# Performance work log

Hardware: AMD Instinct MI355X
Metric: run time of the kernel (lower is better)

The kernel has to match this reference:

```python
import jax, jax.numpy as jnp
import numpy as np

NUM_EMBEDDINGS = 1024
EMBEDDING_DIM = 64


def setup_inputs() -> dict:
    key = jax.random.key(0)
    kx, kw = jax.random.split(key)
    x = jax.random.normal(kx, (16, 4096, EMBEDDING_DIM), dtype=jnp.float32)
    # torch init: uniform(-1/K, 1/K)
    bound = 1.0 / NUM_EMBEDDINGS
    weight = jax.random.uniform(kw, (NUM_EMBEDDINGS, EMBEDDING_DIM),
                                dtype=jnp.float32, minval=-bound, maxval=bound)
    return {"x": x, "weight": weight}


def reference(x, weight):
    flat_x = x.reshape(-1, EMBEDDING_DIM)                      # [N, D]
    x_sq = jnp.sum(flat_x ** 2, axis=1, keepdims=True)
    w_sq = jnp.sum(weight ** 2, axis=1)[None, :]
    distances = x_sq - 2.0 * (flat_x @ weight.T) + w_sq
    encoding_indices = jnp.argmin(distances, axis=1)           # [N]
    quantized = weight[encoding_indices]                       # [N, D]
    e_latent_loss = jnp.mean((jax.lax.stop_gradient(quantized) - flat_x) ** 2)
    q_latent_loss = jnp.mean((quantized - jax.lax.stop_gradient(flat_x)) ** 2)
    loss = q_latent_loss + 0.25 * e_latent_loss
    # straight-through estimator
    quantized = flat_x + jax.lax.stop_gradient(quantized - flat_x)
    return quantized.reshape(x.shape), encoding_indices, loss
```

## Files before the change

kernel.cpp:

```cpp
#include <hip/hip_runtime.h>
#include <math.h>

#define EMB_D 64
#define MARGIN 6.0e-5f
#define SBIAS 0.5f

typedef float  f32x4  __attribute__((ext_vector_type(4)));
typedef short  bf16x8 __attribute__((ext_vector_type(8)));

__device__ __forceinline__ unsigned short f2bf(float f) {
    unsigned int u = __float_as_uint(f);
    return (unsigned short)((u + 0x7FFFu + ((u >> 16) & 1u)) >> 16);
}
__device__ __forceinline__ float bf2f(unsigned short h) {
    return __uint_as_float(((unsigned int)h) << 16);
}

union Pack8 { ushort u[8]; bf16x8 v; uint4 q; };

__device__ __forceinline__ bf16x8 ldbf8(const uint4* p) {
    union { uint4 u; bf16x8 v; } c;
    c.u = *p;
    return c.v;
}

__global__ __launch_bounds__(256)
void vq_prepw_kernel(const float* __restrict__ w,
                     unsigned short* __restrict__ wt_hi,
                     unsigned short* __restrict__ wt_lo,
                     float* __restrict__ wsq, float* __restrict__ loss_out,
                     int K) {
    const int i = blockIdx.x * 256 + threadIdx.x;
    if (i == 0) loss_out[0] = 0.f;
    if (i >= K * 8) return;
    const int krow = i >> 3, q = i & 7;
    const int dest = ((krow >> 6) << 9) + (((krow >> 4) & 3) << 7) + (q << 4)
                   + (krow & 15);
    const float* src = w + (size_t)krow * EMB_D + q * 8;
    Pack8 h, l;
#pragma unroll
    for (int j = 0; j < 8; ++j) {
        const float f = src[j];
        h.u[j] = f2bf(f);
        l.u[j] = f2bf(f - bf2f(h.u[j]));
    }
    ((uint4*)wt_hi)[dest] = h.q;
    ((uint4*)wt_lo)[dest] = l.q;

    if (i < K) {
        const float* wr = w + (size_t)i * EMB_D;
        float r[8];
#pragma unroll
        for (int j = 0; j < 8; ++j) r[j] = __fmul_rn(wr[j], wr[j]);
#pragma unroll
        for (int t = 1; t < 8; ++t)
#pragma unroll
            for (int j = 0; j < 8; ++j)
                r[j] = __fadd_rn(r[j], __fmul_rn(wr[t * 8 + j], wr[t * 8 + j]));
        float a = __fadd_rn(__fadd_rn(r[0], r[1]), __fadd_rn(r[2], r[3]));
        float b = __fadd_rn(__fadd_rn(r[4], r[5]), __fadd_rn(r[6], r[7]));
        wsq[i] = __fadd_rn(a, b);
    }
}

__global__ __launch_bounds__(256, 4)
void vq_fused_kernel(const float* __restrict__ x,
                     const unsigned short* __restrict__ wt_hi,
                     const unsigned short* __restrict__ wt_lo,
                     const float* __restrict__ wsq,
                     const float* __restrict__ w,
                     float* __restrict__ out, float* __restrict__ loss_out,
                     int K, int N, float scale) {
    const int tid  = threadIdx.x;
    const int lane = tid & 63;
    const int wave = tid >> 6;
    const int quad = lane >> 4;
    const int c16  = lane & 15;
    const int rowbase = blockIdx.x * 64 + wave * 16;

    __shared__ float wsq_lds[1024];
    __shared__ unsigned Mp1[4][16][17];
    __shared__ unsigned Mp2[4][16][17];
    __shared__ int kf[64], strow[64], k2row[64];

    const float* xrow = x + (size_t)(rowbase + c16) * EMB_D + quad * 8;
    Pack8 ah0, al0, ah1, al1;
#pragma unroll
    for (int j = 0; j < 8; ++j) {
        const float f0 = xrow[j];
        ah0.u[j] = f2bf(f0); al0.u[j] = f2bf(f0 - bf2f(ah0.u[j]));
        const float f1 = xrow[32 + j];
        ah1.u[j] = f2bf(f1); al1.u[j] = f2bf(f1 - bf2f(ah1.u[j]));
    }
    const bf16x8 AH0 = ah0.v, AL0 = al0.v, AH1 = ah1.v, AL1 = al1.v;

    {
        float4 a = ((const float4*)wsq)[tid];
        a.x += SBIAS; a.y += SBIAS; a.z += SBIAS; a.w += SBIAS;
        ((float4*)wsq_lds)[tid] = a;
    }
    __syncthreads();

    unsigned s1v[4], s2v[4];
#pragma unroll
    for (int i = 0; i < 4; ++i) { s1v[i] = 0xFFFFFFFFu; s2v[i] = 0xFFFFFFFFu; }

    const uint4* gh = (const uint4*)wt_hi;
    const uint4* gl = (const uint4*)wt_lo;

#pragma unroll 4
    for (int u = 0; u < 64; ++u) {
        const int base = u * 128 + lane;
        const bf16x8 bhi0 = ldbf8(gh + base);
        const bf16x8 bhi1 = ldbf8(gh + base + 64);
        const bf16x8 blo0 = ldbf8(gl + base);
        const bf16x8 blo1 = ldbf8(gl + base + 64);
        const float wqb = wsq_lds[u * 16 + c16];

        f32x4 a0 = {0.f, 0.f, 0.f, 0.f};
        f32x4 a1 = {0.f, 0.f, 0.f, 0.f};
        a0 = __builtin_amdgcn_mfma_f32_16x16x32_bf16(AL0, bhi0, a0, 0, 0, 0);
        a1 = __builtin_amdgcn_mfma_f32_16x16x32_bf16(AL1, bhi1, a1, 0, 0, 0);
        a0 = __builtin_amdgcn_mfma_f32_16x16x32_bf16(AH0, blo0, a0, 0, 0, 0);
        a1 = __builtin_amdgcn_mfma_f32_16x16x32_bf16(AH1, blo1, a1, 0, 0, 0);
        a0 = __builtin_amdgcn_mfma_f32_16x16x32_bf16(AH0, bhi0, a0, 0, 0, 0);
        a1 = __builtin_amdgcn_mfma_f32_16x16x32_bf16(AH1, bhi1, a1, 0, 0, 0);
#pragma unroll
        for (int i = 0; i < 4; ++i) {
            const float sc = fmaf(-2.0f, a0[i] + a1[i], wqb);
            const unsigned p = (__float_as_uint(sc) & 0xFFFFFFC0u)
                             | (unsigned)u;
            const unsigned mx = p > s1v[i] ? p : s1v[i];
            s2v[i] = s2v[i] < mx ? s2v[i] : mx;
            s1v[i] = s1v[i] < p  ? s1v[i] : p;
        }
    }

#pragma unroll
    for (int i = 0; i < 4; ++i) {
        Mp1[wave][quad * 4 + i][c16] = s1v[i];
        Mp2[wave][quad * 4 + i][c16] = s2v[i];
    }
    __syncthreads();
    if (tid < 64) {
        const int wv = tid >> 4, r = tid & 15;
        unsigned g1 = 0xFFFFFFFFu, g2 = 0xFFFFFFFFu, g3 = 0xFFFFFFFFu;
        int gk1 = 0, gk2 = 0;
#pragma unroll
        for (int c = 0; c < 16; ++c) {
            {
                const unsigned p = Mp1[wv][r][c];
                if (p < g1)      { g3 = g2; g2 = g1; gk2 = gk1; g1 = p;
                                   gk1 = (int)(((p & 63u) << 4) | (unsigned)c); }
                else if (p < g2) { g3 = g2; g2 = p;
                                   gk2 = (int)(((p & 63u) << 4) | (unsigned)c); }
                else if (p < g3) { g3 = p; }
            }
            {
                const unsigned p = Mp2[wv][r][c];
                if (p < g1)      { g3 = g2; g2 = g1; gk2 = gk1; g1 = p;
                                   gk1 = (int)(((p & 63u) << 4) | (unsigned)c); }
                else if (p < g2) { g3 = g2; g2 = p;
                                   gk2 = (int)(((p & 63u) << 4) | (unsigned)c); }
                else if (p < g3) { g3 = p; }
            }
        }
        kf[tid] = gk1;
        const float f1 = __uint_as_float(g1 & 0xFFFFFFC0u);
        const float f2 = __uint_as_float(g2 & 0xFFFFFFC0u);
        const float f3 = __uint_as_float(g3 & 0xFFFFFFC0u);
        int st = 0;
        if (f2 - f1 <= MARGIN) st = (f3 - f1 > MARGIN) ? 1 : 2;
        strow[tid] = st;
        k2row[tid] = gk2;
    }
    __syncthreads();

    if (tid < 64 && strow[tid] == 1) {
        const int row = blockIdx.x * 64 + tid;
        const int ka = kf[tid], kb = k2row[tid];
        const float4* xp = (const float4*)(x + (size_t)row * EMB_D);
        const float4* wa = (const float4*)(w + (size_t)ka * EMB_D);
        const float4* wb = (const float4*)(w + (size_t)kb * EMB_D);
        float r[8];
        double aa0 = 0, aa1 = 0, aa2 = 0, aa3 = 0;
        double ab0 = 0, ab1 = 0, ab2 = 0, ab3 = 0;
#pragma unroll
        for (int q = 0; q < 16; ++q) {
            const float4 xv = xp[q], va = wa[q], vb = wb[q];
            const int j = (q & 1) * 4;
            if (q < 2) {
                r[j + 0] = __fmul_rn(xv.x, xv.x);
                r[j + 1] = __fmul_rn(xv.y, xv.y);
                r[j + 2] = __fmul_rn(xv.z, xv.z);
                r[j + 3] = __fmul_rn(xv.w, xv.w);
            } else {
                r[j + 0] = __fadd_rn(r[j + 0], __fmul_rn(xv.x, xv.x));
                r[j + 1] = __fadd_rn(r[j + 1], __fmul_rn(xv.y, xv.y));
                r[j + 2] = __fadd_rn(r[j + 2], __fmul_rn(xv.z, xv.z));
                r[j + 3] = __fadd_rn(r[j + 3], __fmul_rn(xv.w, xv.w));
            }
            aa0 = fma((double)xv.x, (double)va.x, aa0);
            aa1 = fma((double)xv.y, (double)va.y, aa1);
            aa2 = fma((double)xv.z, (double)va.z, aa2);
            aa3 = fma((double)xv.w, (double)va.w, aa3);
            ab0 = fma((double)xv.x, (double)vb.x, ab0);
            ab1 = fma((double)xv.y, (double)vb.y, ab1);
            ab2 = fma((double)xv.z, (double)vb.z, ab2);
            ab3 = fma((double)xv.w, (double)vb.w, ab3);
        }
        const float xsq = __fadd_rn(
            __fadd_rn(__fadd_rn(r[0], r[1]), __fadd_rn(r[2], r[3])),
            __fadd_rn(__fadd_rn(r[4], r[5]), __fadd_rn(r[6], r[7])));
        const float mfa = (float)((aa0 + aa1) + (aa2 + aa3));
        const float mfb = (float)((ab0 + ab1) + (ab2 + ab3));
        const float sa = __fadd_rn(__fsub_rn(xsq, __fmul_rn(2.0f, mfa)), wsq[ka]);
        const float sb = __fadd_rn(__fsub_rn(xsq, __fmul_rn(2.0f, mfb)), wsq[kb]);
        int win = ka;
        if (sb < sa || (sb == sa && kb < ka)) win = kb;
        kf[tid] = win;
    }
    __syncthreads();

    __shared__ float4 xs4[16];
    __shared__ float  xsqs;
    __shared__ float  ls[256];
    __shared__ int    lk[256];
    for (int i = 0; i < 64; ++i) {
        if (strow[i] != 2) continue;
        const int row = blockIdx.x * 64 + i;
        if (tid < 16) xs4[tid] = ((const float4*)(x + (size_t)row * EMB_D))[tid];
        __syncthreads();
        if (tid == 0) {
            const float* xf = (const float*)xs4;
            float r[8];
#pragma unroll
            for (int j = 0; j < 8; ++j) r[j] = __fmul_rn(xf[j], xf[j]);
#pragma unroll
            for (int t = 1; t < 8; ++t)
#pragma unroll
                for (int j = 0; j < 8; ++j)
                    r[j] = __fadd_rn(r[j], __fmul_rn(xf[t * 8 + j], xf[t * 8 + j]));
            xsqs = __fadd_rn(
                __fadd_rn(__fadd_rn(r[0], r[1]), __fadd_rn(r[2], r[3])),
                __fadd_rn(__fadd_rn(r[4], r[5]), __fadd_rn(r[6], r[7])));
        }
        __syncthreads();
        const float xsq = xsqs;

        float bs = INFINITY;
        int   bk = K;
        for (int t = 0; t < 4; ++t) {
            const int k = wave * (K >> 2) + t * 64 + lane;
            const float4* wr4 = (const float4*)(w + (size_t)k * EMB_D);
            double a0 = 0.0, a1 = 0.0, a2 = 0.0, a3 = 0.0;
#pragma unroll
            for (int q = 0; q < EMB_D / 4; ++q) {
                const float4 xv = xs4[q];
                const float4 wv = wr4[q];
                a0 = fma((double)xv.x, (double)wv.x, a0);
                a1 = fma((double)xv.y, (double)wv.y, a1);
                a2 = fma((double)xv.z, (double)wv.z, a2);
                a3 = fma((double)xv.w, (double)wv.w, a3);
            }
            const float mf = (float)((a0 + a1) + (a2 + a3));
            const float t2 = __fsub_rn(xsq, __fmul_rn(2.0f, mf));
            const float sc = __fadd_rn(t2, wsq[k]);
            if (sc < bs || (sc == bs && k < bk)) { bs = sc; bk = k; }
        }
        ls[tid] = bs; lk[tid] = bk;
        __syncthreads();
        if (wave == 0) {
            float gs = ls[lane];
            int   gk = lk[lane];
#pragma unroll
            for (int c = 1; c < 4; ++c) {
                const float os = ls[c * 64 + lane];
                const int   ok = lk[c * 64 + lane];
                if (os < gs || (os == gs && ok < gk)) { gs = os; gk = ok; }
            }
#pragma unroll
            for (int off = 32; off > 0; off >>= 1) {
                const float os = __shfl_down(gs, off);
                const int   ok = __shfl_down(gk, off);
                if (os < gs || (os == gs && ok < gk)) { gs = os; gk = ok; }
            }
            if (lane == 0) kf[i] = gk;
        }
        __syncthreads();
    }

    if (tid < 64) {
        const int row = blockIdx.x * 64 + tid;
        out[(size_t)N * EMB_D + row] = (float)kf[tid];
    }
    float lpart = 0.f;
#pragma unroll
    for (int rep = 0; rep < 4; ++rep) {
        int f4   = rep * 256 + tid;
        int rr   = f4 >> 4;
        int c    = f4 & 15;
        int k    = kf[rr];
        int grow = blockIdx.x * 64 + rr;
        float4 wv = ((const float4*)(w + (size_t)k * EMB_D))[c];
        float4 xq = ((const float4*)(x + (size_t)grow * EMB_D))[c];
        ((float4*)out)[(size_t)grow * (EMB_D / 4) + c] = wv;
        float dx = wv.x - xq.x, dy = wv.y - xq.y;
        float dz = wv.z - xq.z, dw = wv.w - xq.w;
        lpart += dx * dx + dy * dy + dz * dz + dw * dw;
    }
#pragma unroll
    for (int off = 32; off > 0; off >>= 1) lpart += __shfl_down(lpart, off);
    __shared__ float lred[4];
    if (lane == 0) lred[wave] = lpart;
    __syncthreads();
    if (tid == 0)
        atomicAdd(loss_out, ((lred[0] + lred[1]) + (lred[2] + lred[3])) * scale);
}

extern "C" void kernel_launch(void* const* d_in, const int* in_sizes, int n_in,
                              void* d_out, int out_size, void* d_ws, size_t ws_size,
                              hipStream_t stream) {
    const float* x = (const float*)d_in[0];
    const float* w = (const float*)d_in[1];
    float* out = (float*)d_out;
    const int xsz = in_sizes[0];
    const int wsz = in_sizes[1];
    const int N   = xsz / EMB_D;
    const int K   = wsz / EMB_D;
    const int NB  = N / 64;
    float* loss_out = out + (size_t)N * EMB_D + N;

    float* wsq = (float*)d_ws;
    unsigned short* wt_hi = (unsigned short*)(wsq + K);
    unsigned short* wt_lo = wt_hi + (size_t)K * EMB_D;

    vq_prepw_kernel<<<(K * 8 + 255) / 256, 256, 0, stream>>>(w, wt_hi, wt_lo,
                                                             wsq, loss_out, K);
    vq_fused_kernel<<<NB, 256, 0, stream>>>(x, wt_hi, wt_lo, wsq, w, out,
                                            loss_out, K, N,
                                            1.25f / (float)xsz);
}
```

Before: 162.8 us.

## Stage codebook tiles in LDS with register-prefetch double buffering

Each of the four waves previously streamed the whole bf16 hi/lo codebook from global memory (L2) on its own. Now the block cooperatively copies 64-code segments into shared memory, and all waves read the MFMA B operands from LDS. The next segment is prefetched into registers while the current one is computed. This cuts redundant global/L2 traffic per block, at the cost of two barriers per segment and about 16KB more LDS, which may reduce occupancy.

```diff
diff --git a/kernel.cpp b/kernel.cpp
--- a/kernel.cpp
+++ b/kernel.cpp
@@ -18,9 +18,9 @@
 
 union Pack8 { ushort u[8]; bf16x8 v; uint4 q; };
 
-__device__ __forceinline__ bf16x8 ldbf8(const uint4* p) {
+__device__ __forceinline__ bf16x8 ldbf8(const unsigned short* p) {
     union { uint4 u; bf16x8 v; } c;
-    c.u = *p;
+    c.u = *(const uint4*)p;
     return c.v;
 }
 
@@ -78,6 +78,8 @@
     const int c16  = lane & 15;
     const int rowbase = blockIdx.x * 64 + wave * 16;
 
+    __shared__ uint4 sh4[512];
+    __shared__ uint4 sl4[512];
     __shared__ float wsq_lds[1024];
     __shared__ unsigned Mp1[4][16][17];
     __shared__ unsigned Mp2[4][16][17];
@@ -99,7 +101,6 @@
         a.x += SBIAS; a.y += SBIAS; a.z += SBIAS; a.w += SBIAS;
         ((float4*)wsq_lds)[tid] = a;
     }
-    __syncthreads();
 
     unsigned s1v[4], s2v[4];
 #pragma unroll
@@ -107,33 +108,49 @@
 
     const uint4* gh = (const uint4*)wt_hi;
     const uint4* gl = (const uint4*)wt_lo;
-
-#pragma unroll 4
-    for (int u = 0; u < 64; ++u) {
-        const int base = u * 128 + lane;
-        const bf16x8 bhi0 = ldbf8(gh + base);
-        const bf16x8 bhi1 = ldbf8(gh + base + 64);
-        const bf16x8 blo0 = ldbf8(gl + base);
-        const bf16x8 blo1 = ldbf8(gl + base + 64);
-        const float wqb = wsq_lds[u * 16 + c16];
-
-        f32x4 a0 = {0.f, 0.f, 0.f, 0.f};
-        f32x4 a1 = {0.f, 0.f, 0.f, 0.f};
-        a0 = __builtin_amdgcn_mfma_f32_16x16x32_bf16(AL0, bhi0, a0, 0, 0, 0);
-        a1 = __builtin_amdgcn_mfma_f32_16x16x32_bf16(AL1, bhi1, a1, 0, 0, 0);
-        a0 = __builtin_amdgcn_mfma_f32_16x16x32_bf16(AH0, blo0, a0, 0, 0, 0);
-        a1 = __builtin_amdgcn_mfma_f32_16x16x32_bf16(AH1, blo1, a1, 0, 0, 0);
-        a0 = __builtin_amdgcn_mfma_f32_16x16x32_bf16(AH0, bhi0, a0, 0, 0, 0);
-        a1 = __builtin_amdgcn_mfma_f32_16x16x32_bf16(AH1, bhi1, a1, 0, 0, 0);
-#pragma unroll
-        for (int i = 0; i < 4; ++i) {
-            const float sc = fmaf(-2.0f, a0[i] + a1[i], wqb);
-            const unsigned p = (__float_as_uint(sc) & 0xFFFFFFC0u)
-                             | (unsigned)u;
-            const unsigned mx = p > s1v[i] ? p : s1v[i];
-            s2v[i] = s2v[i] < mx ? s2v[i] : mx;
-            s1v[i] = s1v[i] < p  ? s1v[i] : p;
-        }
+    uint4 ph0 = gh[tid], ph1 = gh[256 + tid];
+    uint4 pl0 = gl[tid], pl1 = gl[256 + tid];
+
+    const int nseg = K >> 6;
+    for (int seg = 0; seg < nseg; ++seg) {
+        sh4[tid] = ph0; sh4[256 + tid] = ph1;
+        sl4[tid] = pl0; sl4[256 + tid] = pl1;
+        __syncthreads();
+        if (seg + 1 < nseg) {
+            const int b = (seg + 1) * 512;
+            ph0 = gh[b + tid]; ph1 = gh[b + 256 + tid];
+            pl0 = gl[b + tid]; pl1 = gl[b + 256 + tid];
+        }
+
+#pragma unroll
+        for (int s = 0; s < 4; ++s) {
+            const unsigned short* shp = (const unsigned short*)sh4;
+            const unsigned short* slp = (const unsigned short*)sl4;
+            const bf16x8 bhi0 = ldbf8(shp + (s * 128 + lane) * 8);
+            const bf16x8 bhi1 = ldbf8(shp + (s * 128 + 64 + lane) * 8);
+            const bf16x8 blo0 = ldbf8(slp + (s * 128 + lane) * 8);
+            const bf16x8 blo1 = ldbf8(slp + (s * 128 + 64 + lane) * 8);
+            const float wqb = wsq_lds[seg * 64 + s * 16 + c16];
+            const unsigned idx6 = (unsigned)(seg * 4 + s);
+
+            f32x4 a0 = {0.f, 0.f, 0.f, 0.f};
+            f32x4 a1 = {0.f, 0.f, 0.f, 0.f};
+            a0 = __builtin_amdgcn_mfma_f32_16x16x32_bf16(AL0, bhi0, a0, 0, 0, 0);
+            a1 = __builtin_amdgcn_mfma_f32_16x16x32_bf16(AL1, bhi1, a1, 0, 0, 0);
+            a0 = __builtin_amdgcn_mfma_f32_16x16x32_bf16(AH0, blo0, a0, 0, 0, 0);
+            a1 = __builtin_amdgcn_mfma_f32_16x16x32_bf16(AH1, blo1, a1, 0, 0, 0);
+            a0 = __builtin_amdgcn_mfma_f32_16x16x32_bf16(AH0, bhi0, a0, 0, 0, 0);
+            a1 = __builtin_amdgcn_mfma_f32_16x16x32_bf16(AH1, bhi1, a1, 0, 0, 0);
+#pragma unroll
+            for (int i = 0; i < 4; ++i) {
+                const float sc = fmaf(-2.0f, a0[i] + a1[i], wqb);
+                const unsigned p = (__float_as_uint(sc) & 0xFFFFFFC0u) | idx6;
+                const unsigned mx = p > s1v[i] ? p : s1v[i];
+                s2v[i] = s2v[i] < mx ? s2v[i] : mx;
+                s1v[i] = s1v[i] < p  ? s1v[i] : p;
+            }
+        }
+        __syncthreads();
     }
 
 #pragma unroll
```

Result: faster. 157.2 us (-3.4%).
